# Kernel tuning notes

Measured on AMD Instinct MI355X. Metric: run time of the kernel, lower is better.

Reference implementation:

```python
import jax, jax.numpy as jnp
import numpy as np

GRID = 128          # voxel grid extent per axis
KERNELS = [2, 4, 8] # kernel_size == stride pooling scales
B = 4               # number of batches (point clouds)


def _pool_unpool(feats, seg, num_seg):
    # avg-pool over segment then broadcast back to original points
    sums = jax.ops.segment_sum(feats, seg, num_segments=num_seg)
    cnts = jax.ops.segment_sum(jnp.ones((feats.shape[0], 1), feats.dtype), seg, num_segments=num_seg)
    means = sums / jnp.maximum(cnts, 1.0)
    return means[seg]


def setup_inputs() -> dict:
    key = jax.random.key(0)
    k1, k2, k3, k4, k5 = jax.random.split(key, 5)
    N, C, OUT = 1_048_576, 64, 96
    mult = len(KERNELS) + 1
    feats = jax.random.normal(k1, (N, C), jnp.float32)
    coords = jax.random.randint(k2, (N, 3), 0, GRID, jnp.int32)
    batch_idx = jax.random.randint(k3, (N,), 0, B, jnp.int32)
    W = jax.random.normal(k4, (OUT, C * mult), jnp.float32) / np.sqrt(C * mult)
    b = jax.random.normal(k5, (OUT,), jnp.float32) * 0.01
    return {"feats": feats, "coords": coords, "batch_idx": batch_idx, "W": W, "b": b}


def reference(feats, coords, batch_idx, W, b):
    bidx = batch_idx.astype(jnp.int32)
    # i == 0: global average pooling per batch + MinkowskiBroadcast back to points
    cat = [_pool_unpool(feats, bidx, B)]
    # pyramid levels: AvgPool(k, stride=k) then PoolingTranspose(k, stride=k)
    for k in KERNELS:
        s = GRID // k  # pooled grid size per axis
        pc = coords // k
        seg = ((bidx * s + pc[:, 0]) * s + pc[:, 1]) * s + pc[:, 2]
        cat.append(_pool_unpool(feats, seg, B * s * s * s))
    out = jnp.concatenate(cat, axis=1)  # [N, C * (len(KERNELS)+1)]
    return out @ W.T + b                # MinkowskiLinear
```

## Files before the change

kernel.cpp:

```cpp
#include <hip/hip_runtime.h>
#include <stdint.h>


#define N_PTS   1048576
#define NB      4
#define N2SEG   (NB*64*64*64)
#define N4SEG   (NB*32*32*32)
#define N8SEG   (NB*16*16*16)

typedef unsigned int uint;

#define OFF_SUMS2  ((size_t)0)
#define OFF_CNT2   ((size_t)134217728)
#define OFF_SUMS0F ((size_t)138412032)
#define MEMSET_END ((size_t)138413056)
#define OFF_SUMS4  ((size_t)138413056)
#define OFF_MEAN4  ((size_t)155190272)
#define OFF_CNT4   ((size_t)171967488)
#define OFF_SUMS8  ((size_t)172491776)
#define OFF_MEAN8  ((size_t)174588928)
#define OFF_CNT8   ((size_t)176686080)
#define OFF_MEAN0  ((size_t)176751616)
#define OFF_WF     ((size_t)176752640)
#define WS_NEEDED  ((size_t)176801792)

#define D_S2 0u
#define D_C2 ((uint)(OFF_CNT2 / 4))
#define D_M4 ((uint)(OFF_MEAN4 / 4))
#define D_M8 ((uint)(OFF_MEAN8 / 4))
#define D_M0 ((uint)(OFF_MEAN0 / 4))

typedef short s8v __attribute__((ext_vector_type(8)));
typedef float f4v __attribute__((ext_vector_type(4)));
typedef uint  u4v __attribute__((ext_vector_type(4)));

__device__ __forceinline__ uint pack_bf16x2(float a, float b) {
  uint ua = __float_as_uint(a), ub = __float_as_uint(b);
  ua = (ua + 0x7fffu + ((ua >> 16) & 1u)) >> 16;
  ub = (ub + 0x7fffu + ((ub >> 16) & 1u)) >> 16;
  return (ub << 16) | ua;
}
__device__ __forceinline__ float bflo(uint u) { return __uint_as_float(u << 16); }
__device__ __forceinline__ float bfhi(uint u) { return __uint_as_float(u & 0xffff0000u); }

__device__ __forceinline__ uint scale_pk(uint u, float rc) {
  return pack_bf16x2(bflo(u) * rc, bfhi(u) * rc);
}

#define ZERO_U4 (MEMSET_END / 16)
__global__ __launch_bounds__(256) void k_zero(u4v* __restrict__ p) {
  u4v z = (u4v)0u;
  size_t stride = (size_t)gridDim.x * 256;
  for (size_t i = blockIdx.x * 256ull + threadIdx.x; i < ZERO_U4; i += stride)
    __builtin_nontemporal_store(z, &p[i]);
}

__global__ __launch_bounds__(256) void k_wf(const float* __restrict__ W,
                                            uint* __restrict__ Wf) {
  int idx = blockIdx.x * 256 + threadIdx.x;
  int d = idx & 3, l = (idx >> 2) & 63, ktnt = idx >> 8;
  int kt = ktnt / 6, nt = ktnt - kt * 6;
  int n = nt * 16 + (l & 15);
  int k = kt * 32 + (l >> 4) * 8 + d * 2;
  Wf[idx] = pack_bf16x2(W[n * 256 + k], W[n * 256 + k + 1]);
}

__global__ __launch_bounds__(256) void k_scatter2(
    const float* __restrict__ feats, const int* __restrict__ coords,
    const int* __restrict__ batch, uint* __restrict__ sums2,
    uint* __restrict__ cnt2)
{
  int l = threadIdx.x & 63;
  int c2 = l & 31, half = l >> 5;
  int wid = (blockIdx.x * 256 + threadIdx.x) >> 6;
  int nw = (gridDim.x * 256) >> 6;
  for (int p0 = wid * 2; p0 < N_PTS; p0 += nw * 2) {
    int p = p0 + half;
    float2 f = ((const float2*)feats)[(size_t)p * 32 + c2];
    int b = batch[p];
    int x = coords[3 * p], y = coords[3 * p + 1], z = coords[3 * p + 2];
    int s2 = ((b * 64 + (x >> 1)) * 64 + (y >> 1)) * 64 + (z >> 1);
    uint pk = pack_bf16x2(f.x, f.y);
    uint64_t addr = (uint64_t)(uintptr_t)(sums2 + (size_t)s2 * 32 + c2);
    asm volatile("global_atomic_pk_add_bf16 %0, %1, off"
                 :: "v"(addr), "v"(pk));
    if (c2 == 0) atomicAdd(&cnt2[s2], 1u);
  }
}

__global__ __launch_bounds__(256) void k_down_bf(
    const uint* __restrict__ sumsF, const uint* __restrict__ cntF,
    uint* __restrict__ sumsC, uint* __restrict__ meanC,
    uint* __restrict__ cntC, int lgC, int nC)
{
  int tid = blockIdx.x * 256 + threadIdx.x;
  int sc = tid >> 5, c2 = tid & 31;
  if (sc >= nC) return;
  int CG = 1 << lgC, FG = CG << 1;
  int b = sc >> (3 * lgC);
  int r = sc & ((1 << (3 * lgC)) - 1);
  int x = r >> (2 * lgC), y = (r >> lgC) & (CG - 1), z = r & (CG - 1);
  float sx = 0.f, sy = 0.f;
  uint cn = 0;
  #pragma unroll
  for (int dx = 0; dx < 2; ++dx)
    #pragma unroll
    for (int dy = 0; dy < 2; ++dy)
      #pragma unroll
      for (int dz = 0; dz < 2; ++dz) {
        int sf = ((b * FG + 2 * x + dx) * FG + (2 * y + dy)) * FG + (2 * z + dz);
        uint u = sumsF[(size_t)sf * 32 + c2];
        sx += bflo(u); sy += bfhi(u);
        cn += cntF[sf];
      }
  sumsC[(size_t)sc * 32 + c2] = pack_bf16x2(sx, sy);
  float rc = 1.0f / (float)(cn > 1u ? cn : 1u);
  meanC[(size_t)sc * 32 + c2] = pack_bf16x2(sx * rc, sy * rc);
  if (c2 == 0) cntC[sc] = cn;
}

__global__ __launch_bounds__(256) void k_gpart(
    const uint* __restrict__ sums8, float* __restrict__ sums0f)
{
  __shared__ float2 red[8][32];
  int b = blockIdx.x >> 5, chunk = blockIdx.x & 31;
  int t = threadIdx.x, c2 = t & 31, g = t >> 5;
  float sx = 0.f, sy = 0.f;
  for (int i = g; i < 128; i += 8) {
    uint u = sums8[(size_t)(b * 4096 + chunk * 128 + i) * 32 + c2];
    sx += bflo(u); sy += bfhi(u);
  }
  red[g][c2] = make_float2(sx, sy);
  __syncthreads();
  if (g == 0) {
    float ax = 0.f, ay = 0.f;
    #pragma unroll
    for (int i = 0; i < 8; ++i) { ax += red[i][c2].x; ay += red[i][c2].y; }
    unsafeAtomicAdd(&sums0f[b * 64 + 2 * c2], ax);
    unsafeAtomicAdd(&sums0f[b * 64 + 2 * c2 + 1], ay);
  }
}

__global__ __launch_bounds__(256) void k_fin0(
    const float* __restrict__ sums0f, const uint* __restrict__ cnt8,
    uint* __restrict__ mean0)
{
  __shared__ uint redc[256];
  __shared__ float rcs[NB];
  int t = threadIdx.x;
  uint cn = 0;
  for (int i = 0; i < 64; ++i) cn += cnt8[t * 64 + i];
  redc[t] = cn;
  __syncthreads();
  if (t < NB) {
    uint s = 0;
    for (int i = 0; i < 64; ++i) s += redc[t * 64 + i];
    rcs[t] = 1.0f / (float)(s > 1u ? s : 1u);
  }
  __syncthreads();
  if (t < 128) {
    int b = t >> 5, c2 = t & 31;
    float rc = rcs[b];
    mean0[b * 32 + c2] =
        pack_bf16x2(sums0f[b * 64 + 2 * c2] * rc, sums0f[b * 64 + 2 * c2 + 1] * rc);
  }
}

#define GPB 8
__global__ __launch_bounds__(256) void k_final(
    const int* __restrict__ coords, const int* __restrict__ batch,
    const uint* __restrict__ wsb,
    const uint4* __restrict__ Wf, const float* __restrict__ bias,
    float* __restrict__ out)
{
  __shared__ uint4 wf[3072];
  int t = threadIdx.x;
  #pragma unroll
  for (int i = 0; i < 12; ++i) wf[i * 256 + t] = Wf[i * 256 + t];
  int l = t & 63, w = t >> 6, pl = l & 15, q = l >> 4;
  float bn[6];
  #pragma unroll
  for (int nt = 0; nt < 6; ++nt) bn[nt] = bias[nt * 16 + pl];
  __syncthreads();

  uint4 afc[8];
  uint cvc;
  {
    int p = blockIdx.x * (GPB * 64) + w * 16 + pl;
    int b = batch[p];
    int x = coords[3 * p], y = coords[3 * p + 1], z = coords[3 * p + 2];
    int s2 = ((b * 64 + (x >> 1)) * 64 + (y >> 1)) * 64 + (z >> 1);
    int s4 = ((b * 32 + (x >> 2)) * 32 + (y >> 2)) * 32 + (z >> 2);
    int s8 = ((b * 16 + (x >> 3)) * 16 + (y >> 3)) * 16 + (z >> 3);
    const uint4* a0 = (const uint4*)(wsb + D_M0 + b * 32);
    const uint4* a2 = (const uint4*)(wsb + D_S2 + s2 * 32);
    const uint4* a4 = (const uint4*)(wsb + D_M4 + s4 * 32);
    const uint4* a8 = (const uint4*)(wsb + D_M8 + s8 * 32);
    afc[0] = a0[q];     afc[1] = a0[4 + q];
    afc[2] = a2[q];     afc[3] = a2[4 + q];
    afc[4] = a4[q];     afc[5] = a4[4 + q];
    afc[6] = a8[q];     afc[7] = a8[4 + q];
    cvc = wsb[D_C2 + s2];
  }

  #pragma unroll 1
  for (int g = 0; g < GPB; ++g) {
    uint4 afn[8];
    uint cvn = 0;
    if (g + 1 < GPB) {
      int p = blockIdx.x * (GPB * 64) + (g + 1) * 64 + w * 16 + pl;
      int b = batch[p];
      int x = coords[3 * p], y = coords[3 * p + 1], z = coords[3 * p + 2];
      int s2 = ((b * 64 + (x >> 1)) * 64 + (y >> 1)) * 64 + (z >> 1);
      int s4 = ((b * 32 + (x >> 2)) * 32 + (y >> 2)) * 32 + (z >> 2);
      int s8 = ((b * 16 + (x >> 3)) * 16 + (y >> 3)) * 16 + (z >> 3);
      const uint4* a0 = (const uint4*)(wsb + D_M0 + b * 32);
      const uint4* a2 = (const uint4*)(wsb + D_S2 + s2 * 32);
      const uint4* a4 = (const uint4*)(wsb + D_M4 + s4 * 32);
      const uint4* a8 = (const uint4*)(wsb + D_M8 + s8 * 32);
      afn[0] = a0[q];     afn[1] = a0[4 + q];
      afn[2] = a2[q];     afn[3] = a2[4 + q];
      afn[4] = a4[q];     afn[5] = a4[4 + q];
      afn[6] = a8[q];     afn[7] = a8[4 + q];
      cvn = wsb[D_C2 + s2];
    }

    float rc = 1.0f / (float)(cvc > 1u ? cvc : 1u);
    afc[2].x = scale_pk(afc[2].x, rc); afc[2].y = scale_pk(afc[2].y, rc);
    afc[2].z = scale_pk(afc[2].z, rc); afc[2].w = scale_pk(afc[2].w, rc);
    afc[3].x = scale_pk(afc[3].x, rc); afc[3].y = scale_pk(afc[3].y, rc);
    afc[3].z = scale_pk(afc[3].z, rc); afc[3].w = scale_pk(afc[3].w, rc);
    f4v acc[6];
    #pragma unroll
    for (int nt = 0; nt < 6; ++nt) acc[nt] = (f4v)0.0f;
    #pragma unroll
    for (int kt = 0; kt < 8; ++kt) {
      s8v afr = __builtin_bit_cast(s8v, afc[kt]);
      #pragma unroll
      for (int nt = 0; nt < 6; ++nt) {
        s8v bf = __builtin_bit_cast(s8v, wf[(kt * 6 + nt) * 64 + l]);
        acc[nt] = __builtin_amdgcn_mfma_f32_16x16x32_bf16(afr, bf, acc[nt], 0, 0, 0);
      }
    }
    int pbase = blockIdx.x * (GPB * 64) + g * 64 + w * 16;
    float* ob = out + (size_t)(pbase + q * 4) * 96 + pl;
    #pragma unroll
    for (int nt = 0; nt < 6; ++nt)
      #pragma unroll
      for (int r = 0; r < 4; ++r)
        ob[r * 96 + nt * 16] = bn[nt] + acc[nt][r];

    #pragma unroll
    for (int i = 0; i < 8; ++i) afc[i] = afn[i];
    cvc = cvn;
  }
}

extern "C" void kernel_launch(void* const* d_in, const int* in_sizes, int n_in,
                              void* d_out, int out_size, void* d_ws, size_t ws_size,
                              hipStream_t stream)
{
  const float* feats  = (const float*)d_in[0];
  const int*   coords = (const int*)d_in[1];
  const int*   batch  = (const int*)d_in[2];
  const float* W      = (const float*)d_in[3];
  const float* bias   = (const float*)d_in[4];
  float* out = (float*)d_out;
  char* ws = (char*)d_ws;
  if (ws_size < WS_NEEDED) return;

  uint*  sums2  = (uint*)(ws + OFF_SUMS2);
  uint*  cnt2   = (uint*)(ws + OFF_CNT2);
  float* sums0f = (float*)(ws + OFF_SUMS0F);
  uint*  sums4  = (uint*)(ws + OFF_SUMS4);
  uint*  mean4  = (uint*)(ws + OFF_MEAN4);
  uint*  cnt4   = (uint*)(ws + OFF_CNT4);
  uint*  sums8  = (uint*)(ws + OFF_SUMS8);
  uint*  mean8  = (uint*)(ws + OFF_MEAN8);
  uint*  cnt8   = (uint*)(ws + OFF_CNT8);
  uint*  mean0  = (uint*)(ws + OFF_MEAN0);
  uint*  Wf     = (uint*)(ws + OFF_WF);

  k_zero<<<2048, 256, 0, stream>>>((u4v*)ws);
  k_wf<<<48, 256, 0, stream>>>(W, Wf);
  k_scatter2<<<8192, 256, 0, stream>>>(feats, coords, batch, sums2, cnt2);
  k_down_bf<<<(N4SEG * 32) / 256, 256, 0, stream>>>(sums2, cnt2, sums4, mean4, cnt4, 5, N4SEG);
  k_down_bf<<<(N8SEG * 32) / 256, 256, 0, stream>>>(sums4, cnt4, sums8, mean8, cnt8, 4, N8SEG);
  k_gpart<<<128, 256, 0, stream>>>(sums8, sums0f);
  k_fin0<<<1, 256, 0, stream>>>(sums0f, cnt8, mean0);
  k_final<<<N_PTS / (GPB * 64), 256, 0, stream>>>(
      coords, batch, (const uint*)ws, (const uint4*)Wf, bias, out);
}
```

Baseline: 428.2 us.

## Count points first to skip zeroing and atomics for sparse level-2 voxels

```diff
diff --git a/kernel.cpp b/kernel.cpp
--- a/kernel.cpp
+++ b/kernel.cpp
@@ -13,7 +13,8 @@
 #define OFF_SUMS2  ((size_t)0)
 #define OFF_CNT2   ((size_t)134217728)
 #define OFF_SUMS0F ((size_t)138412032)
-#define MEMSET_END ((size_t)138413056)
+#define ZERO_BEG   OFF_CNT2
+#define ZERO_END   ((size_t)138413056)
 #define OFF_SUMS4  ((size_t)138413056)
 #define OFF_MEAN4  ((size_t)155190272)
 #define OFF_CNT4   ((size_t)171967488)
@@ -33,6 +34,7 @@
 typedef short s8v __attribute__((ext_vector_type(8)));
 typedef float f4v __attribute__((ext_vector_type(4)));
 typedef uint  u4v __attribute__((ext_vector_type(4)));
+typedef float f2v __attribute__((ext_vector_type(2)));
 
 __device__ __forceinline__ uint pack_bf16x2(float a, float b) {
   uint ua = __float_as_uint(a), ub = __float_as_uint(b);
@@ -47,12 +49,31 @@
   return pack_bf16x2(bflo(u) * rc, bfhi(u) * rc);
 }
 
-#define ZERO_U4 (MEMSET_END / 16)
-__global__ __launch_bounds__(256) void k_zero(u4v* __restrict__ p) {
+#define ZCNT_U4 ((ZERO_END - ZERO_BEG) / 16)
+__global__ __launch_bounds__(256) void k_zero_cnt(u4v* __restrict__ p) {
   u4v z = (u4v)0u;
   size_t stride = (size_t)gridDim.x * 256;
-  for (size_t i = blockIdx.x * 256ull + threadIdx.x; i < ZERO_U4; i += stride)
+  for (size_t i = blockIdx.x * 256ull + threadIdx.x; i < ZCNT_U4; i += stride)
     __builtin_nontemporal_store(z, &p[i]);
+}
+
+__global__ __launch_bounds__(256) void k_cnt(
+    const int* __restrict__ coords, const int* __restrict__ batch,
+    uint* __restrict__ cnt2)
+{
+  int p = blockIdx.x * 256 + threadIdx.x;
+  int b = batch[p];
+  int x = coords[3 * p], y = coords[3 * p + 1], z = coords[3 * p + 2];
+  int s2 = ((b * 64 + (x >> 1)) * 64 + (y >> 1)) * 64 + (z >> 1);
+  atomicAdd(&cnt2[s2], 1u);
+}
+
+__global__ __launch_bounds__(256) void k_zmulti(
+    const uint* __restrict__ cnt2, u4v* __restrict__ sums2q)
+{
+  int tid = blockIdx.x * 256 + threadIdx.x;
+  int seg = tid >> 3, part = tid & 7;
+  if (cnt2[seg] >= 2u) sums2q[seg * 8 + part] = (u4v)0u;
 }
 
 __global__ __launch_bounds__(256) void k_wf(const float* __restrict__ W,
@@ -68,7 +89,7 @@
 __global__ __launch_bounds__(256) void k_scatter2(
     const float* __restrict__ feats, const int* __restrict__ coords,
     const int* __restrict__ batch, uint* __restrict__ sums2,
-    uint* __restrict__ cnt2)
+    const uint* __restrict__ cnt2)
 {
   int l = threadIdx.x & 63;
   int c2 = l & 31, half = l >> 5;
@@ -76,15 +97,20 @@
   int nw = (gridDim.x * 256) >> 6;
   for (int p0 = wid * 2; p0 < N_PTS; p0 += nw * 2) {
     int p = p0 + half;
-    float2 f = ((const float2*)feats)[(size_t)p * 32 + c2];
+    f2v f = __builtin_nontemporal_load(((const f2v*)feats) + (size_t)p * 32 + c2);
     int b = batch[p];
     int x = coords[3 * p], y = coords[3 * p + 1], z = coords[3 * p + 2];
     int s2 = ((b * 64 + (x >> 1)) * 64 + (y >> 1)) * 64 + (z >> 1);
     uint pk = pack_bf16x2(f.x, f.y);
-    uint64_t addr = (uint64_t)(uintptr_t)(sums2 + (size_t)s2 * 32 + c2);
-    asm volatile("global_atomic_pk_add_bf16 %0, %1, off"
-                 :: "v"(addr), "v"(pk));
-    if (c2 == 0) atomicAdd(&cnt2[s2], 1u);
+    uint cv = cnt2[s2];
+    uint* dst = sums2 + (size_t)s2 * 32 + c2;
+    if (cv == 1u) {
+      *dst = pk;
+    } else {
+      uint64_t addr = (uint64_t)(uintptr_t)dst;
+      asm volatile("global_atomic_pk_add_bf16 %0, %1, off"
+                   :: "v"(addr), "v"(pk));
+    }
   }
 }
 
@@ -109,9 +135,12 @@
       #pragma unroll
       for (int dz = 0; dz < 2; ++dz) {
         int sf = ((b * FG + 2 * x + dx) * FG + (2 * y + dy)) * FG + (2 * z + dz);
-        uint u = sumsF[(size_t)sf * 32 + c2];
-        sx += bflo(u); sy += bfhi(u);
-        cn += cntF[sf];
+        uint cf = cntF[sf];
+        if (cf) {
+          uint u = sumsF[(size_t)sf * 32 + c2];
+          sx += bflo(u); sy += bfhi(u);
+        }
+        cn += cf;
       }
   sumsC[(size_t)sc * 32 + c2] = pack_bf16x2(sx, sy);
   float rc = 1.0f / (float)(cn > 1u ? cn : 1u);
@@ -281,8 +310,10 @@
   uint*  mean0  = (uint*)(ws + OFF_MEAN0);
   uint*  Wf     = (uint*)(ws + OFF_WF);
 
-  k_zero<<<2048, 256, 0, stream>>>((u4v*)ws);
   k_wf<<<48, 256, 0, stream>>>(W, Wf);
+  k_zero_cnt<<<1024, 256, 0, stream>>>((u4v*)(ws + ZERO_BEG));
+  k_cnt<<<N_PTS / 256, 256, 0, stream>>>(coords, batch, cnt2);
+  k_zmulti<<<(N2SEG * 8) / 256, 256, 0, stream>>>(cnt2, (u4v*)sums2);
   k_scatter2<<<8192, 256, 0, stream>>>(feats, coords, batch, sums2, cnt2);
   k_down_bf<<<(N4SEG * 32) / 256, 256, 0, stream>>>(sums2, cnt2, sums4, mean4, cnt4, 5, N4SEG);
   k_down_bf<<<(N8SEG * 32) / 256, 256, 0, stream>>>(sums4, cnt4, sums8, mean8, cnt8, 4, N8SEG);
```

New measurement: 419.0 us. 2.1% less time.
